# Performance work log

Measured on AMD Instinct MI355X. Metric: run time of the kernel, lower is better.

Reference implementation:

```python
import jax, jax.numpy as jnp
import numpy as np

L, B, S, D, H, E, DH, K = 2, 4, 1024, 512, 8, 8, 2048, 2
HEAD = D // H
EPS = 1e-6


def setup_inputs() -> dict:
    key = jax.random.key(0)
    ks = jax.random.split(key, 10)
    s = 0.02
    rn = lambda k, shp: (s * jax.random.normal(k, shp, jnp.float32))
    return {
        "x": jax.random.normal(ks[0], (B, S, D), jnp.float32),
        "ln1_w": jnp.ones((L, D), jnp.float32),
        "ln1_b": jnp.zeros((L, D), jnp.float32),
        "wq": rn(ks[1], (L, D, D)),
        "wk": rn(ks[2], (L, D, D)),
        "wv": rn(ks[3], (L, D, D)),
        "wo": rn(ks[4], (L, D, D)),
        "bo": jnp.zeros((L, D), jnp.float32),
        "ln2_w": jnp.ones((L, D), jnp.float32),
        "ln2_b": jnp.zeros((L, D), jnp.float32),
        "gate_w": rn(ks[5], (L, D, E)),
        "w1": rn(ks[6], (L, E, D, DH)),
        "b1": jnp.zeros((L, E, DH), jnp.float32),
        "w2": rn(ks[7], (L, E, DH, D)),
        "b2": jnp.zeros((L, E, D), jnp.float32),
    }


def _layer_norm(x, w, b):
    mu = jnp.mean(x, axis=-1, keepdims=True)
    var = jnp.mean(jnp.square(x - mu), axis=-1, keepdims=True)
    return (x - mu) * jax.lax.rsqrt(var + EPS) * w + b


def _attention(h, wq_l, wk_l, wv_l, wo_l, bo_l):
    # h: [B,S,D] -> multi-head qk attention (attn_mode='qk'), dropout is eval (identity)
    q = (h @ wq_l).reshape(B, S, H, HEAD)
    k = (h @ wk_l).reshape(B, S, H, HEAD)
    v = (h @ wv_l).reshape(B, S, H, HEAD)
    attn = jnp.einsum('bqhd,bkhd->bhqk', q, k) / np.sqrt(HEAD).astype(np.float32)
    attn = jax.nn.softmax(attn, axis=-1)
    out = jnp.einsum('bhqk,bkhd->bqhd', attn, v).reshape(B, S, D)
    return out @ wo_l + bo_l


def _moe_ffn(x2d, gw, w1_l, b1_l, w2_l, b2_l):
    # x2d: [T,D]; top-k noisy-vmoe gate at eval: clean logits, softmax over the top-k logits
    logits = x2d @ gw  # [T,E]
    topv, topi = jax.lax.top_k(logits, K)  # [T,K]
    gates = jax.nn.softmax(topv, axis=-1)  # [T,K]
    T = x2d.shape[0]
    combine = jnp.zeros((T, E), x2d.dtype).at[jnp.arange(T)[:, None], topi].add(gates)  # [T,E]
    # dense grouped-expert MLP (exact erf GELU as torch.nn.GELU)
    hmid = jax.nn.gelu(jnp.einsum('td,edh->teh', x2d, w1_l) + b1_l[None], approximate=False)
    y = jnp.einsum('teh,ehd->ted', hmid, w2_l) + b2_l[None]
    return jnp.einsum('te,ted->td', combine, y)


def reference(x, ln1_w, ln1_b, wq, wk, wv, wo, bo, ln2_w, ln2_b, gate_w, w1, b1, w2, b2):
    for l in range(L):
        residue = x
        h = _layer_norm(x, ln1_w[l], ln1_b[l])
        x = _attention(h, wq[l], wk[l], wv[l], wo[l], bo[l]) + residue
        residue = x
        h = _layer_norm(x, ln2_w[l], ln2_b[l])
        y = _moe_ffn(h.reshape(B * S, D), gate_w[l], w1[l], b1[l], w2[l], b2[l])
        x = y.reshape(B, S, D) + residue
    return x
```

## Files before the change

kernel.cpp:

```cpp
#include <hip/hip_runtime.h>
#include <cmath>

#define D_MODEL 512
#define T_TOK   4096
#define S_SEQ   1024
#define DH_FF   2048
#define N_EXP   8
#define CAP     9216
#define QKV_LD  1536

typedef __attribute__((ext_vector_type(8))) short bf16x8_t;
typedef __attribute__((ext_vector_type(4))) float f32x4_t;
typedef _Float16 f16x8 __attribute__((ext_vector_type(8)));

__device__ __forceinline__ float gelu_exact(float x) {
    return 0.5f * x * (1.0f + erff(x * 0.70710678118654752440f));
}
__device__ __forceinline__ unsigned short f2bf(float f) {
    union { float f; unsigned int u; } v; v.f = f;
    unsigned int r = v.u + 0x7fff + ((v.u >> 16) & 1);
    return (unsigned short)(r >> 16);
}
__device__ __forceinline__ float bf2f(unsigned short u) {
    union { unsigned int i; float f; } v; v.i = ((unsigned int)u) << 16; return v.f;
}
__device__ __forceinline__ unsigned short f2h(float f) {
    _Float16 h = (_Float16)f;
    return __builtin_bit_cast(unsigned short, h);
}
__device__ __forceinline__ void split1(float v, unsigned short& h, unsigned short& l) {
    _Float16 hf = (_Float16)v;
    _Float16 lf = (_Float16)(v - (float)hf);
    h = __builtin_bit_cast(unsigned short, hf);
    l = __builtin_bit_cast(unsigned short, lf);
}
__device__ __forceinline__ void xcd_swizzle(int& bx, int& by) {
    const int nwg = gridDim.x * gridDim.y;
    const int bid = blockIdx.y * gridDim.x + blockIdx.x;
    const int swz = (bid & 7) * (nwg >> 3) + (bid >> 3);
    bx = swz % gridDim.x;
    by = swz / gridDim.x;
}

__global__ __launch_bounds__(256) void ln_kernel(
    const float* __restrict__ x, const float* __restrict__ w,
    const float* __restrict__ b, float* __restrict__ outf,
    unsigned short* __restrict__ outHi, unsigned short* __restrict__ outLo,
    unsigned short* __restrict__ outb, float* __restrict__ xcopy)
{
    const int t = blockIdx.x, tid = threadIdx.x;
    const float* xr = x + (size_t)t * D_MODEL;
    float v0 = xr[tid], v1 = xr[tid + 256];
    __shared__ float ss[256], sq[256];
    ss[tid] = v0 + v1;
    sq[tid] = v0 * v0 + v1 * v1;
    __syncthreads();
    for (int st = 128; st > 0; st >>= 1) {
        if (tid < st) { ss[tid] += ss[tid + st]; sq[tid] += sq[tid + st]; }
        __syncthreads();
    }
    float mu  = ss[0] * (1.0f / 512.0f);
    float var = sq[0] * (1.0f / 512.0f) - mu * mu;
    float rs  = rsqrtf(var + 1e-6f);
    float o0 = (v0 - mu) * rs * w[tid]       + b[tid];
    float o1 = (v1 - mu) * rs * w[tid + 256] + b[tid + 256];
    if (outf) {
        float* outr = outf + (size_t)t * D_MODEL;
        outr[tid] = o0; outr[tid + 256] = o1;
    }
    if (outHi) {
        unsigned short h0, l0, h1, l1;
        split1(o0, h0, l0); split1(o1, h1, l1);
        unsigned short* oh = outHi + (size_t)t * D_MODEL;
        unsigned short* ol = outLo + (size_t)t * D_MODEL;
        oh[tid] = h0; oh[tid + 256] = h1;
        ol[tid] = l0; ol[tid + 256] = l1;
    }
    if (outb) {
        unsigned short* ob = outb + (size_t)t * D_MODEL;
        ob[tid] = f2bf(o0); ob[tid + 256] = f2bf(o1);
    }
    if (xcopy) {
        float* xc = xcopy + (size_t)t * D_MODEL;
        xc[tid] = v0; xc[tid + 256] = v1;
    }
}

__global__ __launch_bounds__(256) void tconv_split(
    const float* __restrict__ in, int inLd, size_t eStrideIn,
    unsigned short* __restrict__ outHi, unsigned short* __restrict__ outLo,
    int outLd, size_t eStrideOut)
{
    __shared__ float Ts[32][33];
    const int tid = threadIdx.x;
    const int k0 = blockIdx.y * 32, n0 = blockIdx.x * 32;
    in    += (size_t)blockIdx.z * eStrideIn;
    outHi += (size_t)blockIdx.z * eStrideOut;
    outLo += (size_t)blockIdx.z * eStrideOut;
    int r = tid >> 3, c = (tid & 7) * 4;
    float4 v = *(const float4*)&in[(size_t)(k0 + r) * inLd + n0 + c];
    Ts[r][c] = v.x; Ts[r][c + 1] = v.y; Ts[r][c + 2] = v.z; Ts[r][c + 3] = v.w;
    __syncthreads();
    int n = tid >> 3, kk = (tid & 7) * 4;
    ushort4 h4, l4;
    split1(Ts[kk][n],     h4.x, l4.x); split1(Ts[kk + 1][n], h4.y, l4.y);
    split1(Ts[kk + 2][n], h4.z, l4.z); split1(Ts[kk + 3][n], h4.w, l4.w);
    size_t o = (size_t)(n0 + n) * outLd + k0 + kk;
    *(ushort4*)&outHi[o] = h4;
    *(ushort4*)&outLo[o] = l4;
}

__global__ __launch_bounds__(256) void tconv(
    const float* __restrict__ in, int inLd, size_t eStrideIn,
    unsigned short* __restrict__ out, int outLd, size_t eStrideOut)
{
    __shared__ float Ts[32][33];
    const int tid = threadIdx.x;
    const int k0 = blockIdx.y * 32, n0 = blockIdx.x * 32;
    in  += (size_t)blockIdx.z * eStrideIn;
    out += (size_t)blockIdx.z * eStrideOut;
    int r = tid >> 3, c = (tid & 7) * 4;
    float4 v = *(const float4*)&in[(size_t)(k0 + r) * inLd + n0 + c];
    Ts[r][c] = v.x; Ts[r][c + 1] = v.y; Ts[r][c + 2] = v.z; Ts[r][c + 3] = v.w;
    __syncthreads();
    int n = tid >> 3, kk = (tid & 7) * 4;
    ushort4 o;
    o.x = f2bf(Ts[kk][n]);     o.y = f2bf(Ts[kk + 1][n]);
    o.z = f2bf(Ts[kk + 2][n]); o.w = f2bf(Ts[kk + 3][n]);
    *(ushort4*)&out[(size_t)(n0 + n) * outLd + k0 + kk] = o;
}

template<int MODE>
__global__ __launch_bounds__(256) void gemm_pre(
    const unsigned short* __restrict__ Ahi, const unsigned short* __restrict__ Alo,
    int lda, int KLEN,
    const unsigned short* __restrict__ Bhi, const unsigned short* __restrict__ Blo,
    size_t BeStride,
    float* __restrict__ C, int ldc,
    const float* __restrict__ bias, int biasStride,
    const float* __restrict__ resid,
    const int* __restrict__ offs, const int* __restrict__ rowtok, int beta,
    unsigned short* __restrict__ Chi, unsigned short* __restrict__ Clo)
{
    __shared__ unsigned short As_hi[64][40], As_lo[64][40];
    __shared__ unsigned short Bs_hi[64][40], Bs_lo[64][40];
    __shared__ int rt[64];
    __shared__ float rg[64];
    const int tid = threadIdx.x;
    int bx, by;
    xcd_swizzle(bx, by);
    const int row0 = by * 64, col0 = bx * 64;
    int e = 0;
    if (MODE == 2 || MODE == 5) {
        #pragma unroll
        for (int i = 1; i < N_EXP; i++) if (offs[i] <= row0) e = i;
        if (tid < 64) rt[tid] = rowtok[row0 + tid];
        if (MODE == 5 && tid >= 64 && tid < 128) rg[tid - 64] = resid[row0 + tid - 64];
        __syncthreads();
    }
    const unsigned short* BeH = Bhi + (size_t)e * BeStride;
    const unsigned short* BeL = Blo + (size_t)e * BeStride;
    const int lane = tid & 63, w = tid >> 6;
    const int wrow = (w >> 1) * 32, wcol = (w & 1) * 32;
    const int m_ = lane & 15, q_ = lane >> 4;
    f32x4_t acc[2][2];
    #pragma unroll
    for (int i = 0; i < 2; i++)
        #pragma unroll
        for (int j = 0; j < 2; j++) acc[i][j] = (f32x4_t){0.f, 0.f, 0.f, 0.f};

    const int sr = tid >> 2, sc = (tid & 3) * 8;
    size_t arow;
    bool azero = false;
    if (MODE == 2) {
        int t = rt[sr];
        azero = (t < 0);
        arow = (size_t)(azero ? 0 : t) * lda;
    } else {
        arow = (size_t)(row0 + sr) * lda;
    }
    const size_t brow = (size_t)(col0 + sr) * KLEN;

    for (int k0 = 0; k0 < KLEN; k0 += 32) {
        uint4 vh = azero ? make_uint4(0u, 0u, 0u, 0u) : *(const uint4*)&Ahi[arow + k0 + sc];
        uint4 vl = azero ? make_uint4(0u, 0u, 0u, 0u) : *(const uint4*)&Alo[arow + k0 + sc];
        *(uint4*)&As_hi[sr][sc] = vh;
        *(uint4*)&As_lo[sr][sc] = vl;
        *(uint4*)&Bs_hi[sr][sc] = *(const uint4*)&BeH[brow + k0 + sc];
        *(uint4*)&Bs_lo[sr][sc] = *(const uint4*)&BeL[brow + k0 + sc];
        __syncthreads();
        f16x8 ah[2], al[2], bh[2], bl[2];
        #pragma unroll
        for (int i = 0; i < 2; i++) {
            int r = wrow + 16 * i + m_;
            ah[i] = *(const f16x8*)&As_hi[r][q_ * 8];
            al[i] = *(const f16x8*)&As_lo[r][q_ * 8];
        }
        #pragma unroll
        for (int j = 0; j < 2; j++) {
            int r = wcol + 16 * j + m_;
            bh[j] = *(const f16x8*)&Bs_hi[r][q_ * 8];
            bl[j] = *(const f16x8*)&Bs_lo[r][q_ * 8];
        }
        #pragma unroll
        for (int i = 0; i < 2; i++)
            #pragma unroll
            for (int j = 0; j < 2; j++) {
                acc[i][j] = __builtin_amdgcn_mfma_f32_16x16x32_f16(ah[i], bl[j], acc[i][j], 0, 0, 0);
                acc[i][j] = __builtin_amdgcn_mfma_f32_16x16x32_f16(al[i], bh[j], acc[i][j], 0, 0, 0);
                acc[i][j] = __builtin_amdgcn_mfma_f32_16x16x32_f16(ah[i], bh[j], acc[i][j], 0, 0, 0);
            }
        __syncthreads();
    }
    #pragma unroll
    for (int i = 0; i < 2; i++) {
        #pragma unroll
        for (int j = 0; j < 2; j++) {
            #pragma unroll
            for (int r = 0; r < 4; r++) {
                int lr = wrow + 16 * i + q_ * 4 + r;
                int gr = row0 + lr;
                int gc = col0 + wcol + 16 * j + m_;
                float v = acc[i][j][r];
                if (MODE == 5) {
                    int t = rt[lr];
                    if (t >= 0) {
                        float add = beta ? bias[(size_t)e * biasStride + gc] : 0.0f;
                        atomicAdd(&C[(size_t)t * ldc + gc], rg[lr] * (v + add));
                    }
                } else if (MODE == 2) {
                    float g = gelu_exact(v + bias[(size_t)e * biasStride + gc]);
                    unsigned short gh, gl;
                    split1(g, gh, gl);
                    size_t idx = (size_t)gr * ldc + gc;
                    Chi[idx] = gh; Clo[idx] = gl;
                } else {
                    size_t idx = (size_t)gr * ldc + gc;
                    if (MODE == 1) C[idx] = v + bias[gc] + resid[idx];
                    else           C[idx] = v;
                }
            }
        }
    }
}

template<int MODE>
__global__ __launch_bounds__(256) void gemm_pre_bt(
    const unsigned short* __restrict__ A, int lda, int KLEN,
    const unsigned short* __restrict__ Bt, size_t BeStride,
    unsigned short* __restrict__ C, int ldc,
    const float* __restrict__ biasBase, int biasStride,
    const int* __restrict__ offs, const int* __restrict__ rowtok,
    const float* __restrict__ rowgate, float* __restrict__ Cout, int beta)
{
    __shared__ unsigned short As[64][72];
    __shared__ unsigned short Bs[64][72];
    __shared__ int rt[64];
    __shared__ float rg[64];
    const int tid = threadIdx.x;
    int bx, by;
    xcd_swizzle(bx, by);
    const int row0 = by * 64, col0 = bx * 64;
    int e = 0;
    #pragma unroll
    for (int i = 1; i < N_EXP; i++) if (offs[i] <= row0) e = i;
    if (tid < 64) rt[tid] = rowtok[row0 + tid];
    if (MODE == 5 && tid >= 64 && tid < 128) rg[tid - 64] = rowgate[row0 + tid - 64];
    __syncthreads();
    const unsigned short* Be = Bt + (size_t)e * BeStride;
    const int lane = tid & 63, w = tid >> 6;
    const int wrow = (w >> 1) * 32, wcol = (w & 1) * 32;
    const int m_ = lane & 15, q_ = lane >> 4;
    f32x4_t acc[2][2];
    #pragma unroll
    for (int i = 0; i < 2; i++)
        #pragma unroll
        for (int j = 0; j < 2; j++) acc[i][j] = (f32x4_t){0.f, 0.f, 0.f, 0.f};

    const int sr = tid >> 3, sc = (tid & 7) * 8;
    size_t arow0, arow1;
    bool az0 = false, az1 = false;
    {
        int r1 = sr + 32;
        if (MODE == 2) {
            int t0 = rt[sr], t1 = rt[r1];
            az0 = (t0 < 0); az1 = (t1 < 0);
            arow0 = (size_t)(az0 ? 0 : t0) * lda;
            arow1 = (size_t)(az1 ? 0 : t1) * lda;
        } else {
            arow0 = (size_t)(row0 + sr) * lda;
            arow1 = (size_t)(row0 + r1) * lda;
        }
    }
    const size_t brow0 = (size_t)(col0 + sr) * KLEN;
    const size_t brow1 = (size_t)(col0 + sr + 32) * KLEN;

    for (int k0 = 0; k0 < KLEN; k0 += 64) {
        uint4 a0 = az0 ? make_uint4(0u, 0u, 0u, 0u) : *(const uint4*)&A[arow0 + k0 + sc];
        uint4 a1 = az1 ? make_uint4(0u, 0u, 0u, 0u) : *(const uint4*)&A[arow1 + k0 + sc];
        *(uint4*)&As[sr][sc]      = a0;
        *(uint4*)&As[sr + 32][sc] = a1;
        *(uint4*)&Bs[sr][sc]      = *(const uint4*)&Be[brow0 + k0 + sc];
        *(uint4*)&Bs[sr + 32][sc] = *(const uint4*)&Be[brow1 + k0 + sc];
        __syncthreads();
        #pragma unroll
        for (int ks = 0; ks < 2; ks++) {
            bf16x8_t af[2], bfr[2];
            #pragma unroll
            for (int i = 0; i < 2; i++)
                af[i] = *(const bf16x8_t*)&As[wrow + 16 * i + m_][ks * 32 + q_ * 8];
            #pragma unroll
            for (int j = 0; j < 2; j++)
                bfr[j] = *(const bf16x8_t*)&Bs[wcol + 16 * j + m_][ks * 32 + q_ * 8];
            #pragma unroll
            for (int i = 0; i < 2; i++)
                #pragma unroll
                for (int j = 0; j < 2; j++)
                    acc[i][j] = __builtin_amdgcn_mfma_f32_16x16x32_bf16(
                        af[i], bfr[j], acc[i][j], 0, 0, 0);
        }
        __syncthreads();
    }
    #pragma unroll
    for (int i = 0; i < 2; i++) {
        #pragma unroll
        for (int j = 0; j < 2; j++) {
            #pragma unroll
            for (int r = 0; r < 4; r++) {
                int lr = wrow + 16 * i + q_ * 4 + r;
                int gr = row0 + lr;
                int gc = col0 + wcol + 16 * j + m_;
                float v = acc[i][j][r];
                if (MODE == 5) {
                    int t = rt[lr];
                    if (t >= 0) {
                        float add = beta ? biasBase[(size_t)e * biasStride + gc] : 0.0f;
                        atomicAdd(&Cout[(size_t)t * ldc + gc], rg[lr] * (v + add));
                    }
                } else {
                    C[(size_t)gr * ldc + gc] =
                        f2bf(gelu_exact(v + biasBase[(size_t)e * biasStride + gc]));
                }
            }
        }
    }
}

__global__ __launch_bounds__(256) void qkv_prep(
    const float* __restrict__ qkvb, unsigned short* __restrict__ Qh,
    unsigned short* __restrict__ Kh, unsigned short* __restrict__ VTh)
{
    __shared__ float Ts[64][65];
    const int tid = threadIdx.x;
    const int t0 = blockIdx.x * 64, hh = blockIdx.y, b = blockIdx.z;
    const int bh = b * 8 + hh;
    const float* src = qkvb + ((size_t)(b * S_SEQ + t0)) * QKV_LD + hh * 64;
    #pragma unroll
    for (int i = 0; i < 4; i++) {
        int flat = tid + i * 256;
        int r = flat >> 4, c4 = (flat & 15) * 4;
        float4 qv = *(const float4*)&src[(size_t)r * QKV_LD + c4];
        float4 kv = *(const float4*)&src[(size_t)r * QKV_LD + 512 + c4];
        float4 vv = *(const float4*)&src[(size_t)r * QKV_LD + 1024 + c4];
        ushort4 qo, ko;
        qo.x = f2h(qv.x * 0.125f); qo.y = f2h(qv.y * 0.125f);
        qo.z = f2h(qv.z * 0.125f); qo.w = f2h(qv.w * 0.125f);
        ko.x = f2h(kv.x); ko.y = f2h(kv.y); ko.z = f2h(kv.z); ko.w = f2h(kv.w);
        size_t o = ((size_t)bh * S_SEQ + t0 + r) * 64 + c4;
        *(ushort4*)&Qh[o] = qo;
        *(ushort4*)&Kh[o] = ko;
        Ts[r][c4] = vv.x; Ts[r][c4 + 1] = vv.y; Ts[r][c4 + 2] = vv.z; Ts[r][c4 + 3] = vv.w;
    }
    __syncthreads();
    #pragma unroll
    for (int i = 0; i < 4; i++) {
        int flat = tid + i * 256;
        int d = flat >> 4, s4 = (flat & 15) * 4;
        ushort4 vo;
        vo.x = f2h(Ts[s4][d]);     vo.y = f2h(Ts[s4 + 1][d]);
        vo.z = f2h(Ts[s4 + 2][d]); vo.w = f2h(Ts[s4 + 3][d]);
        *(ushort4*)&VTh[((size_t)bh * 64 + d) * S_SEQ + t0 + s4] = vo;
    }
}

__global__ __launch_bounds__(256) void flash_attn_mfma(
    const unsigned short* __restrict__ Qh, const unsigned short* __restrict__ Kh,
    const unsigned short* __restrict__ VTh,
    unsigned short* __restrict__ outHi, unsigned short* __restrict__ outLo)
{
    __shared__ unsigned short Ks[64 * 72];
    __shared__ unsigned short Vt[64 * 72];
    __shared__ unsigned short Ps[64 * 72];
    const int tid = threadIdx.x;
    const int lane = tid & 63, w = tid >> 6;
    const int m_ = lane & 15, q_ = lane >> 4;
    const int hh = blockIdx.y, b = blockIdx.z;
    const int bh = b * 8 + hh;
    const int q0 = blockIdx.x * 64;
    const size_t qbase = ((size_t)bh * S_SEQ + q0) * 64;
    const size_t kbase = (size_t)bh * S_SEQ * 64;
    const size_t vbase = (size_t)bh * 64 * S_SEQ;

    f16x8 qa[2];
    #pragma unroll
    for (int c = 0; c < 2; c++)
        qa[c] = *(const f16x8*)&Qh[qbase + (size_t)(w * 16 + m_) * 64 + c * 32 + q_ * 8];

    float m_run[4], l_run[4];
    f32x4_t acc[4];
    #pragma unroll
    for (int r = 0; r < 4; r++) { m_run[r] = -INFINITY; l_run[r] = 0.0f; }
    #pragma unroll
    for (int oj = 0; oj < 4; oj++) acc[oj] = (f32x4_t){0.f, 0.f, 0.f, 0.f};

    for (int kv0 = 0; kv0 < S_SEQ; kv0 += 64) {
        __syncthreads();
        #pragma unroll
        for (int i = 0; i < 2; i++) {
            int g = tid + i * 256;
            int r = g >> 3, c8 = (g & 7) * 8;
            *(uint4*)&Ks[r * 72 + c8] =
                *(const uint4*)&Kh[kbase + (size_t)(kv0 + r) * 64 + c8];
            *(uint4*)&Vt[r * 72 + c8] =
                *(const uint4*)&VTh[vbase + (size_t)r * S_SEQ + kv0 + c8];
        }
        __syncthreads();
        f32x4_t s[4];
        #pragma unroll
        for (int j = 0; j < 4; j++) s[j] = (f32x4_t){0.f, 0.f, 0.f, 0.f};
        #pragma unroll
        for (int c = 0; c < 2; c++)
            #pragma unroll
            for (int j = 0; j < 4; j++) {
                f16x8 kb = *(const f16x8*)&Ks[(j * 16 + m_) * 72 + c * 32 + q_ * 8];
                s[j] = __builtin_amdgcn_mfma_f32_16x16x32_f16(qa[c], kb, s[j], 0, 0, 0);
            }
        float alpha[4];
        #pragma unroll
        for (int r = 0; r < 4; r++) {
            float rm = fmaxf(fmaxf(s[0][r], s[1][r]), fmaxf(s[2][r], s[3][r]));
            #pragma unroll
            for (int mk = 1; mk < 16; mk <<= 1)
                rm = fmaxf(rm, __shfl_xor(rm, mk));
            float mn = fmaxf(m_run[r], rm);
            alpha[r] = __expf(m_run[r] - mn);
            m_run[r] = mn;
            float ps = 0.0f;
            #pragma unroll
            for (int j = 0; j < 4; j++) {
                float p = __expf(s[j][r] - mn);
                s[j][r] = p;
                ps += p;
            }
            #pragma unroll
            for (int mk = 1; mk < 16; mk <<= 1)
                ps += __shfl_xor(ps, mk);
            l_run[r] = l_run[r] * alpha[r] + ps;
        }
        #pragma unroll
        for (int oj = 0; oj < 4; oj++)
            #pragma unroll
            for (int r = 0; r < 4; r++)
                acc[oj][r] *= alpha[r];
        #pragma unroll
        for (int j = 0; j < 4; j++)
            #pragma unroll
            for (int r = 0; r < 4; r++)
                Ps[(w * 16 + q_ * 4 + r) * 72 + j * 16 + m_] = f2h(s[j][r]);
        __syncthreads();
        #pragma unroll
        for (int c = 0; c < 2; c++) {
            f16x8 pa = *(const f16x8*)&Ps[(w * 16 + m_) * 72 + c * 32 + q_ * 8];
            #pragma unroll
            for (int oj = 0; oj < 4; oj++) {
                f16x8 vb = *(const f16x8*)&Vt[(oj * 16 + m_) * 72 + c * 32 + q_ * 8];
                acc[oj] = __builtin_amdgcn_mfma_f32_16x16x32_f16(pa, vb, acc[oj], 0, 0, 0);
            }
        }
    }
    const size_t obase = ((size_t)b * S_SEQ + q0) * D_MODEL + hh * 64;
    #pragma unroll
    for (int r = 0; r < 4; r++) {
        float inv = 1.0f / l_run[r];
        #pragma unroll
        for (int oj = 0; oj < 4; oj++) {
            float v = acc[oj][r] * inv;
            unsigned short vh, vl;
            split1(v, vh, vl);
            size_t idx = obase + (size_t)(w * 16 + q_ * 4 + r) * D_MODEL + oj * 16 + m_;
            outHi[idx] = vh;
            outLo[idx] = vl;
        }
    }
}

__global__ __launch_bounds__(256) void gate_kernel(
    const float* __restrict__ h, const float* __restrict__ gw,
    int* __restrict__ topi, float* __restrict__ gates)
{
    const int w = threadIdx.x >> 6, lane = threadIdx.x & 63;
    const int t = blockIdx.x * 4 + w;
    const float* hr = h + (size_t)t * D_MODEL;
    float acc[N_EXP] = {};
    for (int d = lane; d < D_MODEL; d += 64) {
        float xv = hr[d];
        const float4 g0 = *(const float4*)&gw[(size_t)d * N_EXP];
        const float4 g1 = *(const float4*)&gw[(size_t)d * N_EXP + 4];
        acc[0] += xv * g0.x; acc[1] += xv * g0.y;
        acc[2] += xv * g0.z; acc[3] += xv * g0.w;
        acc[4] += xv * g1.x; acc[5] += xv * g1.y;
        acc[6] += xv * g1.z; acc[7] += xv * g1.w;
    }
    #pragma unroll
    for (int mk = 1; mk < 64; mk <<= 1) {
        #pragma unroll
        for (int e = 0; e < N_EXP; e++) acc[e] += __shfl_xor(acc[e], mk);
    }
    if (lane == 0) {
        int e0 = 0; float v0 = acc[0];
        #pragma unroll
        for (int e = 1; e < N_EXP; e++) if (acc[e] > v0) { v0 = acc[e]; e0 = e; }
        int e1 = -1; float v1 = -INFINITY;
        #pragma unroll
        for (int e = 0; e < N_EXP; e++) if (e != e0 && acc[e] > v1) { v1 = acc[e]; e1 = e; }
        float g0 = 1.0f / (1.0f + __expf(v1 - v0));
        float g1 = 1.0f - g0;
        topi[2 * t] = e0; topi[2 * t + 1] = e1;
        gates[2 * t] = g0; gates[2 * t + 1] = g1;
    }
}

__global__ __launch_bounds__(1024) void route_kernel(
    const int* __restrict__ topi, const float* __restrict__ gates,
    int* __restrict__ offs, int* __restrict__ rowtok, float* __restrict__ rowgate)
{
    __shared__ int wcnt[16][N_EXP];
    __shared__ int wbase[16][N_EXP];
    __shared__ int offs_s[N_EXP + 1];
    const int tid = threadIdx.x, w = tid >> 6, lane = tid & 63;
    const unsigned long long lt = (1ULL << lane) - 1ULL;

    int mye[8];
    int cnt[N_EXP] = {};
    #pragma unroll
    for (int r = 0; r < 8; r++) {
        int i = w * 512 + r * 64 + lane;
        int e = topi[i];
        mye[r] = e;
        #pragma unroll
        for (int e8 = 0; e8 < N_EXP; e8++) {
            unsigned long long m = __ballot(e == e8);
            cnt[e8] += (int)__popcll(m);
        }
    }
    if (lane == 0) {
        #pragma unroll
        for (int e8 = 0; e8 < N_EXP; e8++) wcnt[w][e8] = cnt[e8];
    }
    __syncthreads();
    if (tid == 0) {
        int off = 0;
        for (int e8 = 0; e8 < N_EXP; e8++) {
            offs_s[e8] = off;
            int c = 0;
            for (int ww = 0; ww < 16; ww++) c += wcnt[ww][e8];
            off += (c + 127) & ~127;
        }
        offs_s[N_EXP] = off;
        for (int e8 = 0; e8 <= N_EXP; e8++) offs[e8] = offs_s[e8];
    }
    __syncthreads();
    if (tid < 128) {
        int ww = tid >> 3, e8 = tid & 7;
        int bse = offs_s[e8];
        for (int w2 = 0; w2 < ww; w2++) bse += wcnt[w2][e8];
        wbase[ww][e8] = bse;
    }
    __syncthreads();
    int base[N_EXP];
    #pragma unroll
    for (int e8 = 0; e8 < N_EXP; e8++) base[e8] = wbase[w][e8];
    #pragma unroll
    for (int r = 0; r < 8; r++) {
        int i = w * 512 + r * 64 + lane;
        int e = mye[r];
        int pos = 0;
        #pragma unroll
        for (int e8 = 0; e8 < N_EXP; e8++) {
            unsigned long long m = __ballot(e == e8);
            if (e == e8) pos = base[e8] + (int)__popcll(m & lt);
            base[e8] += (int)__popcll(m);
        }
        rowtok[pos] = i >> 1;
        rowgate[pos] = gates[i];
    }
}

extern "C" void kernel_launch(void* const* d_in, const int* in_sizes, int n_in,
                              void* d_out, int out_size, void* d_ws, size_t ws_size,
                              hipStream_t stream)
{
    const float* x0    = (const float*)d_in[0];
    const float* ln1w  = (const float*)d_in[1];
    const float* ln1b  = (const float*)d_in[2];
    const float* wq    = (const float*)d_in[3];
    const float* wk    = (const float*)d_in[4];
    const float* wv    = (const float*)d_in[5];
    const float* wo    = (const float*)d_in[6];
    const float* bo    = (const float*)d_in[7];
    const float* ln2w  = (const float*)d_in[8];
    const float* ln2b  = (const float*)d_in[9];
    const float* gatew = (const float*)d_in[10];
    const float* w1    = (const float*)d_in[11];
    const float* b1    = (const float*)d_in[12];
    const float* w2    = (const float*)d_in[13];
    const float* b2    = (const float*)d_in[14];
    float* out = (float*)d_out;

    char* ws = (char*)d_ws;
    const size_t MiB = 1 << 20;
    unsigned short* Qh    = (unsigned short*)(ws + 0);
    unsigned short* Kh    = (unsigned short*)(ws + 4 * MiB);
    unsigned short* h_hi  = (unsigned short*)(ws + 8 * MiB);
    unsigned short* h_lo  = (unsigned short*)(ws + 12 * MiB);
    unsigned short* attn_hi = (unsigned short*)(ws + 8 * MiB);
    unsigned short* attn_lo = (unsigned short*)(ws + 12 * MiB);
    float* qkvb = (float*)(ws + 16 * MiB);
    float* x1   = (float*)(ws + 16 * MiB);
    unsigned short* wqkvT_hi = (unsigned short*)(ws + 40 * MiB);
    unsigned short* wqkvT_lo = (unsigned short*)(ws + 40 * MiB + QKV_LD * D_MODEL * 2);
    unsigned short* VTh   = (unsigned short*)(ws + 40 * MiB);
    unsigned short* woT_hi = (unsigned short*)(ws + 44 * MiB);
    unsigned short* woT_lo = (unsigned short*)(ws + 44 * MiB + D_MODEL * D_MODEL * 2);
    unsigned short* h2_hi = (unsigned short*)(ws + 0);
    unsigned short* h2_lo = (unsigned short*)(ws + 4 * MiB);
    unsigned short* h2b   = (unsigned short*)(ws + 0);
    float* h2 = (float*)(ws + 8 * MiB);
    unsigned short* w1T_hi = (unsigned short*)(ws + 8 * MiB);
    unsigned short* w1T_lo = (unsigned short*)(ws + 12 * MiB);
    unsigned short* w2T_hi = (unsigned short*)(ws + 16 * MiB);
    unsigned short* w2T_lo = (unsigned short*)(ws + 20 * MiB);
    unsigned short* hmid_hi = (unsigned short*)(ws + 24 * MiB);
    unsigned short* hmid_lo = (unsigned short*)(ws + 33 * MiB);
    unsigned short* w1T_bf  = (unsigned short*)(ws + 8 * MiB);
    unsigned short* w2T_bf  = (unsigned short*)(ws + 16 * MiB);
    unsigned short* hmidb   = (unsigned short*)(ws + 24 * MiB);
    size_t oI = 46 * MiB;
    int*   topi    = (int*)(ws + oI);
    float* gates   = (float*)(ws + oI + 2 * T_TOK * 4);
    int*   rowtok  = (int*)(ws + oI + 4 * T_TOK * 4);
    float* rowgate = (float*)(ws + oI + 4 * T_TOK * 4 + CAP * 4);
    int*   offs    = (int*)(ws + oI + 4 * T_TOK * 4 + 2 * CAP * 4);
    float* x2 = out;

    const dim3 gW(16, 16, 1);
    const dim3 gW8(16, 16, 8);
    const dim3 gQKV(QKV_LD / 64, T_TOK / 64);
    const dim3 gO(D_MODEL / 64, T_TOK / 64);
    const dim3 gUp1(8, CAP / 64);
    const dim3 gDn1(D_MODEL / 64, CAP / 64);
    const dim3 gUp2(16, CAP / 64);
    const dim3 gDn2(D_MODEL / 64, CAP / 64);
    const dim3 gAttn(S_SEQ / 64, 8, 4);

    for (int l = 0; l < 2; l++) {
        const float* xin = (l == 0) ? x0 : x2;
        float* xout = (l == 1) ? out : x2;
        const float* wq_l = wq + (size_t)l * D_MODEL * D_MODEL;
        const float* wk_l = wk + (size_t)l * D_MODEL * D_MODEL;
        const float* wv_l = wv + (size_t)l * D_MODEL * D_MODEL;
        const float* wo_l = wo + (size_t)l * D_MODEL * D_MODEL;
        const float* w1_l = w1 + (size_t)l * N_EXP * D_MODEL * DH_FF;
        const float* w2_l = w2 + (size_t)l * N_EXP * DH_FF * D_MODEL;
        const float* b1_l = b1 + (size_t)l * N_EXP * DH_FF;
        const float* b2_l = b2 + (size_t)l * N_EXP * D_MODEL;

        ln_kernel<<<T_TOK, 256, 0, stream>>>(xin, ln1w + (size_t)l * D_MODEL,
                                             ln1b + (size_t)l * D_MODEL,
                                             nullptr, h_hi, h_lo, nullptr, nullptr);
        tconv_split<<<gW, 256, 0, stream>>>(wq_l, D_MODEL, 0, wqkvT_hi, wqkvT_lo, D_MODEL, 0);
        tconv_split<<<gW, 256, 0, stream>>>(wk_l, D_MODEL, 0,
                                            wqkvT_hi + 512 * 512, wqkvT_lo + 512 * 512,
                                            D_MODEL, 0);
        tconv_split<<<gW, 256, 0, stream>>>(wv_l, D_MODEL, 0,
                                            wqkvT_hi + 1024 * 512, wqkvT_lo + 1024 * 512,
                                            D_MODEL, 0);
        tconv_split<<<gW, 256, 0, stream>>>(wo_l, D_MODEL, 0, woT_hi, woT_lo, D_MODEL, 0);
        gemm_pre<0><<<gQKV, 256, 0, stream>>>(h_hi, h_lo, D_MODEL, D_MODEL,
                                              wqkvT_hi, wqkvT_lo, 0,
                                              qkvb, QKV_LD, nullptr, 0, nullptr,
                                              nullptr, nullptr, 0, nullptr, nullptr);
        qkv_prep<<<gAttn, 256, 0, stream>>>(qkvb, Qh, Kh, VTh);
        flash_attn_mfma<<<gAttn, 256, 0, stream>>>(Qh, Kh, VTh, attn_hi, attn_lo);
        gemm_pre<1><<<gO, 256, 0, stream>>>(attn_hi, attn_lo, D_MODEL, D_MODEL,
                                            woT_hi, woT_lo, 0,
                                            x1, D_MODEL, bo + (size_t)l * D_MODEL, 0,
                                            xin, nullptr, nullptr, 0, nullptr, nullptr);
        ln_kernel<<<T_TOK, 256, 0, stream>>>(x1, ln2w + (size_t)l * D_MODEL,
                                             ln2b + (size_t)l * D_MODEL, h2,
                                             (l == 0) ? h2_hi : nullptr,
                                             (l == 0) ? h2_lo : nullptr,
                                             (l == 1) ? h2b : nullptr, xout);

        hipMemsetAsync(rowtok, 0xFF, CAP * 4, stream);
        gate_kernel<<<T_TOK / 4, 256, 0, stream>>>(h2, gatew + (size_t)l * D_MODEL * N_EXP,
                                                   topi, gates);
        route_kernel<<<1, 1024, 0, stream>>>(topi, gates, offs, rowtok, rowgate);

        if (l == 0) {
            for (int c = 0; c < 4; c++) {
                tconv_split<<<gW8, 256, 0, stream>>>(w1_l + (size_t)c * 512, DH_FF,
                                                     (size_t)D_MODEL * DH_FF,
                                                     w1T_hi, w1T_lo, D_MODEL,
                                                     (size_t)512 * D_MODEL);
                gemm_pre<2><<<gUp1, 256, 0, stream>>>(h2_hi, h2_lo, D_MODEL, D_MODEL,
                                                      w1T_hi, w1T_lo, (size_t)512 * D_MODEL,
                                                      nullptr, 512,
                                                      b1_l + (size_t)c * 512, DH_FF,
                                                      nullptr, offs, rowtok, 0,
                                                      hmid_hi, hmid_lo);
                tconv_split<<<gW8, 256, 0, stream>>>(w2_l + (size_t)c * 512 * D_MODEL,
                                                     D_MODEL, (size_t)DH_FF * D_MODEL,
                                                     w2T_hi, w2T_lo, 512,
                                                     (size_t)D_MODEL * 512);
                gemm_pre<5><<<gDn1, 256, 0, stream>>>(hmid_hi, hmid_lo, 512, 512,
                                                      w2T_hi, w2T_lo, (size_t)D_MODEL * 512,
                                                      xout, D_MODEL, b2_l, D_MODEL,
                                                      rowgate, offs, rowtok,
                                                      (c == 0) ? 1 : 0, nullptr, nullptr);
            }
        } else {
            for (int c = 0; c < 2; c++) {
                tconv<<<dim3(32, 16, 8), 256, 0, stream>>>(
                    w1_l + (size_t)c * 1024, DH_FF, (size_t)D_MODEL * DH_FF,
                    w1T_bf, D_MODEL, (size_t)1024 * D_MODEL);
                gemm_pre_bt<2><<<gUp2, 256, 0, stream>>>(h2b, D_MODEL, D_MODEL,
                                                         w1T_bf, (size_t)1024 * D_MODEL,
                                                         hmidb, 1024,
                                                         b1_l + (size_t)c * 1024, DH_FF,
                                                         offs, rowtok, nullptr, nullptr, 0);
                tconv<<<dim3(16, 32, 8), 256, 0, stream>>>(
                    w2_l + (size_t)c * 1024 * D_MODEL, D_MODEL, (size_t)DH_FF * D_MODEL,
                    w2T_bf, 1024, (size_t)D_MODEL * 1024);
                gemm_pre_bt<5><<<gDn2, 256, 0, stream>>>(hmidb, 1024, 1024,
                                                         w2T_bf, (size_t)D_MODEL * 1024,
                                                         nullptr, D_MODEL, b2_l, D_MODEL,
                                                         offs, rowtok, rowgate, xout,
                                                         (c == 0) ? 1 : 0);
            }
        }
    }
}
```

Before: 884.4 us.

## Split attention KV range into two segments and batch weight conversion launches

Flash attention now runs two blocks per query tile, each covering half the key range, and writes unnormalized partial outputs plus running max and sum. A new combine kernel merges them and produces the hi/lo split output. The goal is to double the block count (512 to 1024) so the GPU fills better. Separately, the four projection weight conversions are merged into one launch, and the w1/w2 MoE conversions into one launch per chunk, to cut launch count. The split adds fp32 partial-output traffic and one extra kernel. The partial-output buffer must also not overlap live workspace regions.

After: 873.3 us. No clear change (-1.3%).

```diff
diff --git a/kernel.cpp b/kernel.cpp
--- a/kernel.cpp
+++ b/kernel.cpp
@@ -86,17 +86,50 @@
     }
 }
 
-__global__ __launch_bounds__(256) void tconv_split(
-    const float* __restrict__ in, int inLd, size_t eStrideIn,
-    unsigned short* __restrict__ outHi, unsigned short* __restrict__ outLo,
-    int outLd, size_t eStrideOut)
+__global__ __launch_bounds__(256) void tconv_split_proj(
+    const float* __restrict__ wqp, const float* __restrict__ wkp,
+    const float* __restrict__ wvp, const float* __restrict__ wop,
+    unsigned short* __restrict__ qkvHi, unsigned short* __restrict__ qkvLo,
+    unsigned short* __restrict__ oHi, unsigned short* __restrict__ oLo)
 {
     __shared__ float Ts[32][33];
     const int tid = threadIdx.x;
+    const int z = blockIdx.z;
+    const float* in = (z == 0) ? wqp : (z == 1) ? wkp : (z == 2) ? wvp : wop;
+    unsigned short* outHi = (z < 3) ? qkvHi + (size_t)z * 512 * 512 : oHi;
+    unsigned short* outLo = (z < 3) ? qkvLo + (size_t)z * 512 * 512 : oLo;
     const int k0 = blockIdx.y * 32, n0 = blockIdx.x * 32;
-    in    += (size_t)blockIdx.z * eStrideIn;
-    outHi += (size_t)blockIdx.z * eStrideOut;
-    outLo += (size_t)blockIdx.z * eStrideOut;
+    int r = tid >> 3, c = (tid & 7) * 4;
+    float4 v = *(const float4*)&in[(size_t)(k0 + r) * D_MODEL + n0 + c];
+    Ts[r][c] = v.x; Ts[r][c + 1] = v.y; Ts[r][c + 2] = v.z; Ts[r][c + 3] = v.w;
+    __syncthreads();
+    int n = tid >> 3, kk = (tid & 7) * 4;
+    ushort4 h4, l4;
+    split1(Ts[kk][n],     h4.x, l4.x); split1(Ts[kk + 1][n], h4.y, l4.y);
+    split1(Ts[kk + 2][n], h4.z, l4.z); split1(Ts[kk + 3][n], h4.w, l4.w);
+    size_t o = (size_t)(n0 + n) * D_MODEL + k0 + kk;
+    *(ushort4*)&outHi[o] = h4;
+    *(ushort4*)&outLo[o] = l4;
+}
+
+__global__ __launch_bounds__(256) void tconv_split_moe(
+    const float* __restrict__ w1c, const float* __restrict__ w2c,
+    unsigned short* __restrict__ w1Hi, unsigned short* __restrict__ w1Lo,
+    unsigned short* __restrict__ w2Hi, unsigned short* __restrict__ w2Lo)
+{
+    __shared__ float Ts[32][33];
+    const int tid = threadIdx.x;
+    const int z = blockIdx.z, e = z & 7, which = z >> 3;
+    const float* in; int inLd;
+    unsigned short *outHi, *outLo;
+    if (which == 0) {
+        in = w1c + (size_t)e * D_MODEL * DH_FF; inLd = DH_FF;
+        outHi = w1Hi + (size_t)e * 512 * 512; outLo = w1Lo + (size_t)e * 512 * 512;
+    } else {
+        in = w2c + (size_t)e * DH_FF * D_MODEL; inLd = D_MODEL;
+        outHi = w2Hi + (size_t)e * 512 * 512; outLo = w2Lo + (size_t)e * 512 * 512;
+    }
+    const int k0 = blockIdx.y * 32, n0 = blockIdx.x * 32;
     int r = tid >> 3, c = (tid & 7) * 4;
     float4 v = *(const float4*)&in[(size_t)(k0 + r) * inLd + n0 + c];
     Ts[r][c] = v.x; Ts[r][c + 1] = v.y; Ts[r][c + 2] = v.z; Ts[r][c + 3] = v.w;
@@ -105,20 +138,29 @@
     ushort4 h4, l4;
     split1(Ts[kk][n],     h4.x, l4.x); split1(Ts[kk + 1][n], h4.y, l4.y);
     split1(Ts[kk + 2][n], h4.z, l4.z); split1(Ts[kk + 3][n], h4.w, l4.w);
-    size_t o = (size_t)(n0 + n) * outLd + k0 + kk;
+    size_t o = (size_t)(n0 + n) * 512 + k0 + kk;
     *(ushort4*)&outHi[o] = h4;
     *(ushort4*)&outLo[o] = l4;
 }
 
-__global__ __launch_bounds__(256) void tconv(
-    const float* __restrict__ in, int inLd, size_t eStrideIn,
-    unsigned short* __restrict__ out, int outLd, size_t eStrideOut)
+__global__ __launch_bounds__(256) void tconv_moe_bf(
+    const float* __restrict__ w1c, const float* __restrict__ w2c,
+    unsigned short* __restrict__ w1T, unsigned short* __restrict__ w2T)
 {
     __shared__ float Ts[32][33];
     const int tid = threadIdx.x;
-    const int k0 = blockIdx.y * 32, n0 = blockIdx.x * 32;
-    in  += (size_t)blockIdx.z * eStrideIn;
-    out += (size_t)blockIdx.z * eStrideOut;
+    const int z = blockIdx.z, e = z & 7, which = z >> 3;
+    const float* in; int inLd, k0, n0, outLd;
+    unsigned short* out;
+    if (which == 0) {
+        in = w1c + (size_t)e * D_MODEL * DH_FF; inLd = DH_FF;
+        out = w1T + (size_t)e * 1024 * D_MODEL; outLd = D_MODEL;
+        n0 = blockIdx.x * 32; k0 = blockIdx.y * 32;
+    } else {
+        in = w2c + (size_t)e * DH_FF * D_MODEL; inLd = D_MODEL;
+        out = w2T + (size_t)e * D_MODEL * 1024; outLd = 1024;
+        k0 = blockIdx.x * 32; n0 = blockIdx.y * 32;
+    }
     int r = tid >> 3, c = (tid & 7) * 4;
     float4 v = *(const float4*)&in[(size_t)(k0 + r) * inLd + n0 + c];
     Ts[r][c] = v.x; Ts[r][c + 1] = v.y; Ts[r][c + 2] = v.z; Ts[r][c + 3] = v.w;
@@ -386,7 +428,7 @@
 __global__ __launch_bounds__(256) void flash_attn_mfma(
     const unsigned short* __restrict__ Qh, const unsigned short* __restrict__ Kh,
     const unsigned short* __restrict__ VTh,
-    unsigned short* __restrict__ outHi, unsigned short* __restrict__ outLo)
+    float* __restrict__ oP, float* __restrict__ mP, float* __restrict__ lP)
 {
     __shared__ unsigned short Ks[64 * 72];
     __shared__ unsigned short Vt[64 * 72];
@@ -396,7 +438,8 @@
     const int m_ = lane & 15, q_ = lane >> 4;
     const int hh = blockIdx.y, b = blockIdx.z;
     const int bh = b * 8 + hh;
-    const int q0 = blockIdx.x * 64;
+    const int q0 = (blockIdx.x >> 1) * 64;
+    const int seg = blockIdx.x & 1;
     const size_t qbase = ((size_t)bh * S_SEQ + q0) * 64;
     const size_t kbase = (size_t)bh * S_SEQ * 64;
     const size_t vbase = (size_t)bh * 64 * S_SEQ;
@@ -413,7 +456,8 @@
     #pragma unroll
     for (int oj = 0; oj < 4; oj++) acc[oj] = (f32x4_t){0.f, 0.f, 0.f, 0.f};
 
-    for (int kv0 = 0; kv0 < S_SEQ; kv0 += 64) {
+    const int kvEnd = seg * 512 + 512;
+    for (int kv0 = seg * 512; kv0 < kvEnd; kv0 += 64) {
         __syncthreads();
         #pragma unroll
         for (int i = 0; i < 2; i++) {
@@ -478,19 +522,56 @@
             }
         }
     }
-    const size_t obase = ((size_t)b * S_SEQ + q0) * D_MODEL + hh * 64;
+    const size_t pbase = (((size_t)seg * 32 + bh) * S_SEQ + q0) * 64;
     #pragma unroll
     for (int r = 0; r < 4; r++) {
-        float inv = 1.0f / l_run[r];
-        #pragma unroll
-        for (int oj = 0; oj < 4; oj++) {
-            float v = acc[oj][r] * inv;
-            unsigned short vh, vl;
-            split1(v, vh, vl);
-            size_t idx = obase + (size_t)(w * 16 + q_ * 4 + r) * D_MODEL + oj * 16 + m_;
-            outHi[idx] = vh;
-            outLo[idx] = vl;
-        }
+        int row = w * 16 + q_ * 4 + r;
+        #pragma unroll
+        for (int oj = 0; oj < 4; oj++)
+            oP[pbase + (size_t)row * 64 + oj * 16 + m_] = acc[oj][r];
+        if (m_ == 0) {
+            size_t mi = ((size_t)seg * 32 + bh) * S_SEQ + q0 + row;
+            mP[mi] = m_run[r];
+            lP[mi] = l_run[r];
+        }
+    }
+}
+
+__global__ __launch_bounds__(256) void attn_combine(
+    const float* __restrict__ oP, const float* __restrict__ mP,
+    const float* __restrict__ lP,
+    unsigned short* __restrict__ outHi, unsigned short* __restrict__ outLo)
+{
+    const int tid = threadIdx.x;
+    const int hh = blockIdx.y, b = blockIdx.z;
+    const int bh = b * 8 + hh;
+    const int q0 = blockIdx.x * 64;
+    const int r = tid >> 2, c0 = (tid & 3) * 16;
+    const int s = q0 + r;
+    const size_t segO = (size_t)32 * S_SEQ * 64;
+    const size_t segM = (size_t)32 * S_SEQ;
+    const size_t b0 = ((size_t)bh * S_SEQ + s) * 64 + c0;
+    const size_t mi = (size_t)bh * S_SEQ + s;
+    float m0 = mP[mi], m1 = mP[segM + mi];
+    float l0 = lP[mi], l1 = lP[segM + mi];
+    float mm = fmaxf(m0, m1);
+    float e0 = __expf(m0 - mm), e1 = __expf(m1 - mm);
+    float inv = 1.0f / (l0 * e0 + l1 * e1);
+    e0 *= inv; e1 *= inv;
+    const size_t obase = ((size_t)b * S_SEQ + s) * D_MODEL + hh * 64 + c0;
+    #pragma unroll
+    for (int q = 0; q < 4; q++) {
+        float4 v0 = *(const float4*)&oP[b0 + 4 * q];
+        float4 v1 = *(const float4*)&oP[segO + b0 + 4 * q];
+        float o0 = v0.x * e0 + v1.x * e1;
+        float o1 = v0.y * e0 + v1.y * e1;
+        float o2 = v0.z * e0 + v1.z * e1;
+        float o3 = v0.w * e0 + v1.w * e1;
+        ushort4 h4, l4;
+        split1(o0, h4.x, l4.x); split1(o1, h4.y, l4.y);
+        split1(o2, h4.z, l4.z); split1(o3, h4.w, l4.w);
+        *(ushort4*)&outHi[obase + 4 * q] = h4;
+        *(ushort4*)&outLo[obase + 4 * q] = l4;
     }
 }
 
@@ -627,6 +708,9 @@
     unsigned short* attn_lo = (unsigned short*)(ws + 12 * MiB);
     float* qkvb = (float*)(ws + 16 * MiB);
     float* x1   = (float*)(ws + 16 * MiB);
+    float* oPart = (float*)(ws + 16 * MiB);
+    float* mPart = (float*)(ws + 33 * MiB);
+    float* lPart = (float*)(ws + 33 * MiB + 512 * 1024);
     unsigned short* wqkvT_hi = (unsigned short*)(ws + 40 * MiB);
     unsigned short* wqkvT_lo = (unsigned short*)(ws + 40 * MiB + QKV_LD * D_MODEL * 2);
     unsigned short* VTh   = (unsigned short*)(ws + 40 * MiB);
@@ -653,15 +737,18 @@
     int*   offs    = (int*)(ws + oI + 4 * T_TOK * 4 + 2 * CAP * 4);
     float* x2 = out;
 
-    const dim3 gW(16, 16, 1);
-    const dim3 gW8(16, 16, 8);
+    const dim3 gWproj(16, 16, 4);
+    const dim3 gWmoe(16, 16, 16);
+    const dim3 gWmoe2(32, 16, 16);
     const dim3 gQKV(QKV_LD / 64, T_TOK / 64);
     const dim3 gO(D_MODEL / 64, T_TOK / 64);
     const dim3 gUp1(8, CAP / 64);
     const dim3 gDn1(D_MODEL / 64, CAP / 64);
     const dim3 gUp2(16, CAP / 64);
     const dim3 gDn2(D_MODEL / 64, CAP / 64);
-    const dim3 gAttn(S_SEQ / 64, 8, 4);
+    const dim3 gAttnF(2 * S_SEQ / 64, 8, 4);
+    const dim3 gAttnC(S_SEQ / 64, 8, 4);
+    const dim3 gPrep(S_SEQ / 64, 8, 4);
 
     for (int l = 0; l < 2; l++) {
         const float* xin = (l == 0) ? x0 : x2;
@@ -678,20 +765,15 @@
         ln_kernel<<<T_TOK, 256, 0, stream>>>(xin, ln1w + (size_t)l * D_MODEL,
                                              ln1b + (size_t)l * D_MODEL,
                                              nullptr, h_hi, h_lo, nullptr, nullptr);
-        tconv_split<<<gW, 256, 0, stream>>>(wq_l, D_MODEL, 0, wqkvT_hi, wqkvT_lo, D_MODEL, 0);
-        tconv_split<<<gW, 256, 0, stream>>>(wk_l, D_MODEL, 0,
-                                            wqkvT_hi + 512 * 512, wqkvT_lo + 512 * 512,
-                                            D_MODEL, 0);
-        tconv_split<<<gW, 256, 0, stream>>>(wv_l, D_MODEL, 0,
-                                            wqkvT_hi + 1024 * 512, wqkvT_lo + 1024 * 512,
-                                            D_MODEL, 0);
-        tconv_split<<<gW, 256, 0, stream>>>(wo_l, D_MODEL, 0, woT_hi, woT_lo, D_MODEL, 0);
+        tconv_split_proj<<<gWproj, 256, 0, stream>>>(wq_l, wk_l, wv_l, wo_l,
+                                                     wqkvT_hi, wqkvT_lo, woT_hi, woT_lo);
         gemm_pre<0><<<gQKV, 256, 0, stream>>>(h_hi, h_lo, D_MODEL, D_MODEL,
                                               wqkvT_hi, wqkvT_lo, 0,
                                               qkvb, QKV_LD, nullptr, 0, nullptr,
                                               nullptr, nullptr, 0, nullptr, nullptr);
-        qkv_prep<<<gAttn, 256, 0, stream>>>(qkvb, Qh, Kh, VTh);
-        flash_attn_mfma<<<gAttn, 256, 0, stream>>>(Qh, Kh, VTh, attn_hi, attn_lo);
+        qkv_prep<<<gPrep, 256, 0, stream>>>(qkvb, Qh, Kh, VTh);
+        flash_attn_mfma<<<gAttnF, 256, 0, stream>>>(Qh, Kh, VTh, oPart, mPart, lPart);
+        attn_combine<<<gAttnC, 256, 0, stream>>>(oPart, mPart, lPart, attn_hi, attn_lo);
         gemm_pre<1><<<gO, 256, 0, stream>>>(attn_hi, attn_lo, D_MODEL, D_MODEL,
                                             woT_hi, woT_lo, 0,
                                             x1, D_MODEL, bo + (size_t)l * D_MODEL, 0,
@@ -709,20 +791,15 @@
 
         if (l == 0) {
             for (int c = 0; c < 4; c++) {
-                tconv_split<<<gW8, 256, 0, stream>>>(w1_l + (size_t)c * 512, DH_FF,
-                                                     (size_t)D_MODEL * DH_FF,
-                                                     w1T_hi, w1T_lo, D_MODEL,
-                                                     (size_t)512 * D_MODEL);
+                tconv_split_moe<<<gWmoe, 256, 0, stream>>>(
+                    w1_l + (size_t)c * 512, w2_l + (size_t)c * 512 * D_MODEL,
+                    w1T_hi, w1T_lo, w2T_hi, w2T_lo);
                 gemm_pre<2><<<gUp1, 256, 0, stream>>>(h2_hi, h2_lo, D_MODEL, D_MODEL,
                                                       w1T_hi, w1T_lo, (size_t)512 * D_MODEL,
                                                       nullptr, 512,
                                                       b1_l + (size_t)c * 512, DH_FF,
                                                       nullptr, offs, rowtok, 0,
                                                       hmid_hi, hmid_lo);
-                tconv_split<<<gW8, 256, 0, stream>>>(w2_l + (size_t)c * 512 * D_MODEL,
-                                                     D_MODEL, (size_t)DH_FF * D_MODEL,
-                                                     w2T_hi, w2T_lo, 512,
-                                                     (size_t)D_MODEL * 512);
                 gemm_pre<5><<<gDn1, 256, 0, stream>>>(hmid_hi, hmid_lo, 512, 512,
                                                       w2T_hi, w2T_lo, (size_t)D_MODEL * 512,
                                                       xout, D_MODEL, b2_l, D_MODEL,
@@ -731,17 +808,14 @@
             }
         } else {
             for (int c = 0; c < 2; c++) {
-                tconv<<<dim3(32, 16, 8), 256, 0, stream>>>(
-                    w1_l + (size_t)c * 1024, DH_FF, (size_t)D_MODEL * DH_FF,
-                    w1T_bf, D_MODEL, (size_t)1024 * D_MODEL);
+                tconv_moe_bf<<<gWmoe2, 256, 0, stream>>>(
+                    w1_l + (size_t)c * 1024, w2_l + (size_t)c * 1024 * D_MODEL,
+                    w1T_bf, w2T_bf);
                 gemm_pre_bt<2><<<gUp2, 256, 0, stream>>>(h2b, D_MODEL, D_MODEL,
                                                          w1T_bf, (size_t)1024 * D_MODEL,
                                                          hmidb, 1024,
                                                          b1_l + (size_t)c * 1024, DH_FF,
                                                          offs, rowtok, nullptr, nullptr, 0);
-                tconv<<<dim3(16, 32, 8), 256, 0, stream>>>(
-                    w2_l + (size_t)c * 1024 * D_MODEL, D_MODEL, (size_t)DH_FF * D_MODEL,
-                    w2T_bf, 1024, (size_t)D_MODEL * 1024);
                 gemm_pre_bt<5><<<gDn2, 256, 0, stream>>>(hmidb, 1024, 1024,
                                                          w2T_bf, (size_t)D_MODEL * 1024,
                                                          nullptr, D_MODEL, b2_l, D_MODEL,
```
